# Kernel optimization log

Measured on AMD Instinct MI355X. Metric: run time of the kernel, lower is better.

Reference implementation:

```python
import jax, jax.numpy as jnp
import numpy as np

N_ROWS = 8_388_608  # candidate rows
N_VARS = 8          # variable_end


def setup_inputs() -> dict:
    key = jax.random.key(0)
    inputs = jax.random.normal(key, (N_ROWS, N_VARS), dtype=jnp.float32)
    return {"inputs": inputs}


def reference(inputs):
    # Expression tree (prefix seq [11,8,9,8,9,0,1,12,2,13,15,14,3,10,4,8,9,5,5,13,6,7]):
    # tanh( (x0*x1 + sin(x2)) * exp(-|x3|) + x4 / (x5*x5 + exp(x6)) - x7 )
    x0, x1, x2, x3 = inputs[:, 0], inputs[:, 1], inputs[:, 2], inputs[:, 3]
    x4, x5, x6, x7 = inputs[:, 4], inputs[:, 5], inputs[:, 6], inputs[:, 7]
    expr = (x0 * x1 + jnp.sin(x2)) * jnp.exp(-jnp.abs(x3)) \
        + x4 / (x5 * x5 + jnp.exp(x6)) - x7
    return jnp.tanh(expr)
```

## Files before the change

### kernel.cpp

```cpp
#include <hip/hip_runtime.h>
#include <math.h>


typedef float v4f __attribute__((ext_vector_type(4)));

__device__ __forceinline__ float fast_rcp(float x) {
    return __builtin_amdgcn_rcpf(x);
}

__device__ __forceinline__ float fast_tanh(float x) {
    float a = fabsf(x);
    float e = __expf(-2.0f * a);
    float r = fast_rcp(1.0f + e);
    float t = __builtin_fmaf(-(e + e), r, 1.0f);
    return copysignf(t, x);
}

__device__ __forceinline__ float row_expr(v4f a, v4f b) {
    float s   = __sinf(a[2]);
    float e3  = __expf(-fabsf(a[3]));
    float t1  = __builtin_fmaf(a[0], a[1], s) * e3;
    float den = __builtin_fmaf(b[1], b[1], __expf(b[2]));
    float t2  = b[0] * fast_rcp(den);
    return fast_tanh(t1 + t2 - b[3]);
}

__global__ __launch_bounds__(256) void Expression_82643760709953_kernel(
    const v4f* __restrict__ in4, float* __restrict__ out, int n_rows) {
    const int tid = blockIdx.x * blockDim.x + threadIdx.x;
    const int nth = gridDim.x * blockDim.x;
    const int stride = 4 * nth;

    int r = 4 * tid;
    for (; r + 3 < n_rows; r += stride) {
        const v4f* p = &in4[2 * r];
        v4f a0 = __builtin_nontemporal_load(&p[0]);
        v4f b0 = __builtin_nontemporal_load(&p[1]);
        v4f a1 = __builtin_nontemporal_load(&p[2]);
        v4f b1 = __builtin_nontemporal_load(&p[3]);
        v4f a2 = __builtin_nontemporal_load(&p[4]);
        v4f b2 = __builtin_nontemporal_load(&p[5]);
        v4f a3 = __builtin_nontemporal_load(&p[6]);
        v4f b3 = __builtin_nontemporal_load(&p[7]);
        v4f o;
        o[0] = row_expr(a0, b0);
        o[1] = row_expr(a1, b1);
        o[2] = row_expr(a2, b2);
        o[3] = row_expr(a3, b3);
        __builtin_nontemporal_store(o, (v4f*)&out[r]);
    }
    if (r < n_rows) {
        for (int t = r; t < n_rows; ++t) {
            v4f a = __builtin_nontemporal_load(&in4[2 * t]);
            v4f b = __builtin_nontemporal_load(&in4[2 * t + 1]);
            out[t] = row_expr(a, b);
        }
    }
}

extern "C" void kernel_launch(void* const* d_in, const int* in_sizes, int n_in,
                              void* d_out, int out_size, void* d_ws, size_t ws_size,
                              hipStream_t stream) {
    const v4f* in4 = (const v4f*)d_in[0];
    float* out = (float*)d_out;
    int n_rows = out_size;
    int block = 256;
    long quads = ((long)n_rows + 3) / 4;
    long need = (quads + block - 1) / block;
    int grid = (int)(need < 2048 ? need : 2048);
    if (grid < 1) grid = 1;
    Expression_82643760709953_kernel<<<grid, block, 0, stream>>>(in4, out, n_rows);
}
```

Measured before the change: 404.8 us.

## Use wave-coalesced row loads with lane shuffles and a larger grid

Each wavefront now handles a chunk of 64 rows and loads two fully contiguous 1 KiB vec4 blocks, so every load instruction is coalesced. Lane-pair xor shuffles then rebuild each row's two halves, and each lane writes one scalar output. The old scheme had each thread read 128 contiguous bytes at a large per-lane stride. The grid cap rises to 32768 blocks and the nontemporal hints are dropped. In exchange it adds shuffle instructions, scalar 4-byte stores in place of vec4 stores, and less work per thread.

```diff
diff --git a/kernel.cpp b/kernel.cpp
--- a/kernel.cpp
+++ b/kernel.cpp
@@ -27,34 +27,35 @@
 
 __global__ __launch_bounds__(256) void Expression_82643760709953_kernel(
     const v4f* __restrict__ in4, float* __restrict__ out, int n_rows) {
-    const int tid = blockIdx.x * blockDim.x + threadIdx.x;
-    const int nth = gridDim.x * blockDim.x;
-    const int stride = 4 * nth;
+    const int lane   = threadIdx.x & 63;
+    const int wib    = threadIdx.x >> 6;
+    const long gwave = (long)blockIdx.x * (blockDim.x >> 6) + wib;
+    const long nwave = (long)gridDim.x * (blockDim.x >> 6);
+    const long nchunk = (long)n_rows >> 6;
 
-    int r = 4 * tid;
-    for (; r + 3 < n_rows; r += stride) {
-        const v4f* p = &in4[2 * r];
-        v4f a0 = __builtin_nontemporal_load(&p[0]);
-        v4f b0 = __builtin_nontemporal_load(&p[1]);
-        v4f a1 = __builtin_nontemporal_load(&p[2]);
-        v4f b1 = __builtin_nontemporal_load(&p[3]);
-        v4f a2 = __builtin_nontemporal_load(&p[4]);
-        v4f b2 = __builtin_nontemporal_load(&p[5]);
-        v4f a3 = __builtin_nontemporal_load(&p[6]);
-        v4f b3 = __builtin_nontemporal_load(&p[7]);
-        v4f o;
-        o[0] = row_expr(a0, b0);
-        o[1] = row_expr(a1, b1);
-        o[2] = row_expr(a2, b2);
-        o[3] = row_expr(a3, b3);
-        __builtin_nontemporal_store(o, (v4f*)&out[r]);
+    for (long c = gwave; c < nchunk; c += nwave) {
+        const long b4 = c << 7;
+        v4f v0 = in4[b4 + lane];
+        v4f v1 = in4[b4 + 64 + lane];
+        v4f sel = (lane & 1) ? v0 : v1;
+        v4f rcv;
+        rcv[0] = __shfl_xor(sel[0], 1);
+        rcv[1] = __shfl_xor(sel[1], 1);
+        rcv[2] = __shfl_xor(sel[2], 1);
+        rcv[3] = __shfl_xor(sel[3], 1);
+        v4f a = (lane & 1) ? rcv : v0;
+        v4f b = (lane & 1) ? v1  : rcv;
+        long row = (c << 6) + ((long)(lane & 1) << 5) + (lane >> 1);
+        out[row] = row_expr(a, b);
     }
-    if (r < n_rows) {
-        for (int t = r; t < n_rows; ++t) {
-            v4f a = __builtin_nontemporal_load(&in4[2 * t]);
-            v4f b = __builtin_nontemporal_load(&in4[2 * t + 1]);
-            out[t] = row_expr(a, b);
-        }
+
+    const long done = nchunk << 6;
+    const long gtid = (long)blockIdx.x * blockDim.x + threadIdx.x;
+    const long nthr = (long)gridDim.x * blockDim.x;
+    for (long t = done + gtid; t < n_rows; t += nthr) {
+        v4f a = in4[2 * t];
+        v4f b = in4[2 * t + 1];
+        out[t] = row_expr(a, b);
     }
 }
 
@@ -65,9 +66,10 @@
     float* out = (float*)d_out;
     int n_rows = out_size;
     int block = 256;
-    long quads = ((long)n_rows + 3) / 4;
-    long need = (quads + block - 1) / block;
-    int grid = (int)(need < 2048 ? need : 2048);
+    long nchunk = ((long)n_rows + 63) >> 6;
+    long wpb = block >> 6;
+    long need = (nchunk + wpb - 1) / wpb;
+    int grid = (int)(need < 32768 ? need : 32768);
     if (grid < 1) grid = 1;
     Expression_82643760709953_kernel<<<grid, block, 0, stream>>>(in4, out, n_rows);
 }
```

After: 354.9 us. 1.14x faster.
